# Performance work log

Hardware: AMD Instinct MI355X
Metric: run time of the kernel (lower is better)

The kernel has to match this reference:

```python
import jax, jax.numpy as jnp
import numpy as np
import math


def l1_cdist(a, b):
    """L1 pairwise distance sum_d |a_i - b_j| without materializing (..,n,m,d).
    a: (..., n, d), b: (..., m, d) -> (..., n, m). Scans over feature dim."""
    aT = jnp.moveaxis(a, -1, 0)  # (d, ..., n)
    bT = jnp.moveaxis(b, -1, 0)  # (d, ..., m)
    init = jnp.zeros(a.shape[:-1] + (b.shape[-2],), a.dtype)

    def body(acc, ab):
        ai, bi = ab
        return acc + jnp.abs(ai[..., :, None] - bi[..., None, :]), None

    return jax.lax.scan(body, init, (aT, bT))[0]


def sq_l2_cdist(a, b):
    """Squared euclidean pairwise distance via GEMM (matches cdist(p=2)**2, clamped >=0)."""
    a2 = jnp.sum(a * a, axis=-1)
    b2 = jnp.sum(b * b, axis=-1)
    ab = jnp.einsum('...nd,...md->...nm', a, b)
    return jnp.maximum(a2[..., :, None] + b2[..., None, :] - 2.0 * ab, 0.0)


def proxy_delta_linear(x, weight, gain):
    """ProxyDeltaLinearV68 forward. x: (B,T,Din), weight: (Dout,Din), gain: (1,Dout,1)."""
    B, T, Din = x.shape
    Dout = weight.shape[0]
    x_act = jnp.tanh(x).reshape(-1, Din)   # (B*T, Din)
    w_act = jnp.tanh(weight)               # (Dout, Din)
    l1_mean = jax.lax.stop_gradient(l1_cdist(x_act, w_act)) / Din
    l2_sq_mean = sq_l2_cdist(x_act, w_act) / Din
    # (l1 - l2).detach() + l2
    dist = jax.lax.stop_gradient(l1_mean - l2_sq_mean) + l2_sq_mean
    out = (1.0 - dist).reshape(B, T, Dout)
    return (out - 0.5) * gain.reshape(1, 1, Dout)


def attention_forward(x, mask, wq_weight, wq_gain, wk_weight, wk_gain,
                      wv_weight, wv_gain, wo_weight, wo_bias, gamma, rho):
    B, T, C = x.shape
    H = gamma.shape[1]
    d = C // H
    scale = math.sqrt(d)

    q = jnp.tanh(proxy_delta_linear(x, wq_weight, wq_gain))
    k = jnp.tanh(proxy_delta_linear(x, wk_weight, wk_gain))
    v = proxy_delta_linear(x, wv_weight, wv_gain)

    q = q.reshape(B, T, H, d).transpose(0, 2, 1, 3).reshape(B * H, T, d)
    k = k.reshape(B, T, H, d).transpose(0, 2, 1, 3).reshape(B * H, T, d)
    v = v.reshape(B, T, H, d).transpose(0, 2, 1, 3)  # (B,H,T,d)

    l1_mean = jax.lax.stop_gradient(l1_cdist(q, k)) / d       # (B*H,T,T)
    l2_sq_mean = sq_l2_cdist(q, k) / d
    dist_proxy = jax.lax.stop_gradient(l1_mean - l2_sq_mean) + l2_sq_mean
    dist_proxy = dist_proxy.reshape(B, H, T, T)

    dist_scaled = dist_proxy * scale
    dist_final_sq = dist_scaled * dist_scaled
    gamma_pos = jax.nn.softplus(gamma)  # (1,H,1,1)
    rho_pos = jax.nn.softplus(rho)
    base_kernel = 1.0 / (1.0 + gamma_pos * dist_final_sq + 1e-6)
    attn_weights = base_kernel ** rho_pos
    attn_weights = jnp.where(mask == 0, 0.0, attn_weights)
    attn_probs = attn_weights / (jnp.sum(attn_weights, axis=-1, keepdims=True) + 1e-6)

    out = jnp.einsum('bhqk,bhkd->bhqd', attn_probs, v)
    out = out.transpose(0, 2, 1, 3).reshape(B, T, C)
    return out @ wo_weight.T + wo_bias


def setup_inputs() -> dict:
    B, T, C, H = 2, 2048, 512, 8
    key = jax.random.key(0)
    ks = jax.random.split(key, 8)
    x = jax.random.normal(ks[0], (B, T, C), dtype=jnp.float32)
    mask = jnp.tril(jnp.ones((T, T), dtype=jnp.int32))[None, None]  # causal (1,1,T,T)
    mk = lambda k: jax.random.normal(k, (C, C), dtype=jnp.float32) * 0.1
    return {
        'x': x,
        'mask': mask,
        'wq_weight': mk(ks[1]), 'wq_gain': jnp.full((1, C, 1), 2.0, jnp.float32),
        'wk_weight': mk(ks[2]), 'wk_gain': jnp.full((1, C, 1), 2.0, jnp.float32),
        'wv_weight': mk(ks[3]), 'wv_gain': jnp.full((1, C, 1), 2.0, jnp.float32),
        'wo_weight': jax.random.normal(ks[4], (C, C), dtype=jnp.float32) * (1.0 / math.sqrt(C)),
        'wo_bias': jnp.zeros((C,), dtype=jnp.float32),
        'gamma': jnp.ones((1, H, 1, 1), dtype=jnp.float32),
        'rho': jnp.full((1, H, 1, 1), 2.0, jnp.float32),
    }


def reference(x, mask, wq_weight, wq_gain, wk_weight, wk_gain,
              wv_weight, wv_gain, wo_weight, wo_bias, gamma, rho):
    return attention_forward(x, mask, wq_weight, wq_gain, wk_weight, wk_gain,
                             wv_weight, wv_gain, wo_weight, wo_bias, gamma, rho)
```

## Files before the change

kernel.cpp:

```cpp
#include <hip/hip_runtime.h>
#include <hip/hip_bf16.h>

#define T_SEQ 2048
#define CDIM 512
#define HDIM 8
#define DHEAD 64
#define BT 4096

__global__ __launch_bounds__(256) void tanh_prep(
    const float* __restrict__ x,  const float* __restrict__ wq,
    const float* __restrict__ wk, const float* __restrict__ wv,
    float* __restrict__ xact, float* __restrict__ wqa,
    float* __restrict__ wka,  float* __restrict__ wva)
{
    const int NX = BT * CDIM / 4;
    const int NW = CDIM * CDIM / 4;
    int idx = blockIdx.x * 256 + threadIdx.x;
    const float4* src; float4* dst; int off;
    if (idx < NX)           { src = (const float4*)x;  dst = (float4*)xact; off = idx; }
    else if (idx < NX+NW)   { src = (const float4*)wq; dst = (float4*)wqa;  off = idx - NX; }
    else if (idx < NX+2*NW) { src = (const float4*)wk; dst = (float4*)wka;  off = idx - NX - NW; }
    else                    { src = (const float4*)wv; dst = (float4*)wva;  off = idx - NX - 2*NW; }
    float4 t = src[off];
    t.x = tanhf(t.x); t.y = tanhf(t.y); t.z = tanhf(t.z); t.w = tanhf(t.w);
    dst[off] = t;
}

#define PSTR 36
__global__ __launch_bounds__(256) void proj_l1(
    const float* __restrict__ xact,
    const float* __restrict__ wqa, const float* __restrict__ wka, const float* __restrict__ wva,
    const float* __restrict__ gq,  const float* __restrict__ gk,  const float* __restrict__ gv,
    float* __restrict__ oq, float* __restrict__ okk, float* __restrict__ ov)
{
    __shared__ float As[64][PSTR];
    __shared__ float Bs[128][PSTR];

    const int z = blockIdx.z;
    const float* w    = (z == 0) ? wqa : (z == 1) ? wka : wva;
    const float* gain = (z == 0) ? gq  : (z == 1) ? gk  : gv;
    float* outp       = (z == 0) ? oq  : (z == 1) ? okk : ov;

    const int row0 = blockIdx.y * 64;
    const int col0 = blockIdx.x * 128;
    const int tid = threadIdx.x;
    const int tx = tid & 15, ty = tid >> 4;

    float acc[4][8];
    #pragma unroll
    for (int i = 0; i < 4; ++i)
        #pragma unroll
        for (int j = 0; j < 8; ++j) acc[i][j] = 0.f;

    for (int k0 = 0; k0 < CDIM; k0 += 32) {
        float4 av[2], bv[4];
        #pragma unroll
        for (int q = 0; q < 2; ++q) {
            const int fi = tid + 256 * q;
            av[q] = *(const float4*)&xact[(size_t)(row0 + (fi >> 3)) * CDIM + k0 + 4*(fi & 7)];
        }
        #pragma unroll
        for (int q = 0; q < 4; ++q) {
            const int fi = tid + 256 * q;
            bv[q] = *(const float4*)&w[(size_t)(col0 + (fi >> 3)) * CDIM + k0 + 4*(fi & 7)];
        }
        __syncthreads();
        #pragma unroll
        for (int q = 0; q < 2; ++q) {
            const int fi = tid + 256 * q;
            *(float4*)&As[fi >> 3][4*(fi & 7)] = av[q];
        }
        #pragma unroll
        for (int q = 0; q < 4; ++q) {
            const int fi = tid + 256 * q;
            *(float4*)&Bs[fi >> 3][4*(fi & 7)] = bv[q];
        }
        __syncthreads();

        #pragma unroll 2
        for (int kk = 0; kk < 32; kk += 4) {
            float4 a4[4], b4[8];
            #pragma unroll
            for (int i = 0; i < 4; ++i) a4[i] = *(const float4*)&As[ty + 16*i][kk];
            #pragma unroll
            for (int j = 0; j < 8; ++j) b4[j] = *(const float4*)&Bs[tx + 16*j][kk];
            #pragma unroll
            for (int i = 0; i < 4; ++i)
                #pragma unroll
                for (int j = 0; j < 8; ++j)
                    acc[i][j] += fabsf(a4[i].x - b4[j].x) + fabsf(a4[i].y - b4[j].y)
                               + fabsf(a4[i].z - b4[j].z) + fabsf(a4[i].w - b4[j].w);
        }
        __syncthreads();
    }

    float gcol[8];
    #pragma unroll
    for (int j = 0; j < 8; ++j) gcol[j] = gain[col0 + tx + 16*j];

    #pragma unroll
    for (int i = 0; i < 4; ++i) {
        const int r = row0 + ty + 16*i;
        #pragma unroll
        for (int j = 0; j < 8; ++j) {
            const int c = col0 + tx + 16*j;
            float val = (0.5f - acc[i][j] * (1.0f / 512.0f)) * gcol[j];
            if (z < 2) val = tanhf(val);
            outp[(size_t)r * CDIM + c] = val;
        }
    }
}

__global__ __launch_bounds__(256) void attn_l1(
    const float* __restrict__ qg, const float* __restrict__ kg, const float* __restrict__ vg,
    const float* __restrict__ gamma, const float* __restrict__ rho,
    float* __restrict__ slabv, float* __restrict__ slabs)
{
    __shared__ float Qs[128][68];
    __shared__ float Ks[128][68];
    __shared__ float Vs[128][68];
    __shared__ float Ws[128][36];

    const int bh = blockIdx.x;
    const int b = bh >> 3, h = bh & 7;

    int slot = blockIdx.y;
    int s = 15, c = 0;
    for (;; --s) {
        const int nc = (s >> 2) + 1;
        if (slot < nc) { c = slot; break; }
        slot -= nc;
    }
    const int i0 = s * 128;
    const int kt0 = 4 * c;
    const int kt1 = min(4 * c + 3, s);

    const int tid = threadIdx.x;
    const int tx = tid & 15, ty = tid >> 4;
    const int gr = tid >> 3;
    const int gc = (tid & 7) * 4;

    const float gp = log1pf(__expf(gamma[h]));
    const float rp = log1pf(__expf(rho[h]));
    const float gp64 = gp * (1.0f / 64.0f);
    const float mrho = -rp;

    const size_t hb = (size_t)b * T_SEQ * CDIM + h * DHEAD;

    #pragma unroll
    for (int p = 0; p < 4; ++p)
        #pragma unroll
        for (int h2 = 0; h2 < 2; ++h2)
            *(float4*)&Qs[gr + 32*p][gc + 32*h2] =
                *(const float4*)&qg[hb + (size_t)(i0 + gr + 32*p) * CDIM + gc + 32*h2];

    float4 o4[8];
    float accs[8];
    float l1w[8][8];
    #pragma unroll
    for (int i = 0; i < 8; ++i) {
        o4[i] = make_float4(0.f, 0.f, 0.f, 0.f);
        accs[i] = 0.f;
    }

    for (int kt = kt0; kt <= kt1; ++kt) {
        const int j0 = kt * 128;
        __syncthreads();
        #pragma unroll
        for (int p = 0; p < 4; ++p)
            #pragma unroll
            for (int h2 = 0; h2 < 2; ++h2) {
                const size_t off = hb + (size_t)(j0 + gr + 32*p) * CDIM + gc + 32*h2;
                *(float4*)&Ks[gr + 32*p][gc + 32*h2] = *(const float4*)&kg[off];
                *(float4*)&Vs[gr + 32*p][gc + 32*h2] = *(const float4*)&vg[off];
            }
        __syncthreads();

        #pragma unroll
        for (int i = 0; i < 8; ++i)
            #pragma unroll
            for (int j = 0; j < 8; ++j) l1w[i][j] = 0.f;

        #pragma unroll 2
        for (int d0 = 0; d0 < DHEAD; d0 += 4) {
            float4 a4[8];
            #pragma unroll
            for (int i = 0; i < 8; ++i) a4[i] = *(const float4*)&Qs[ty + 16*i][d0];
            #pragma unroll
            for (int j = 0; j < 8; ++j) {
                const float4 kx = *(const float4*)&Ks[tx + 16*j][d0];
                #pragma unroll
                for (int i = 0; i < 8; ++i)
                    l1w[i][j] += fabsf(a4[i].x - kx.x) + fabsf(a4[i].y - kx.y)
                               + fabsf(a4[i].z - kx.z) + fabsf(a4[i].w - kx.w);
            }
        }

        const bool diag = (kt == s);
        #pragma unroll
        for (int i = 0; i < 8; ++i)
            #pragma unroll
            for (int j = 0; j < 8; ++j) {
                const float l1 = l1w[i][j];
                const float den = fmaf(gp64 * l1, l1, 1.000001f);
                float wgt = __builtin_amdgcn_exp2f(mrho * __builtin_amdgcn_logf(den));
                if (diag && (tx + 16*j) > (ty + 16*i)) wgt = 0.f;
                l1w[i][j] = wgt;
                accs[i] += wgt;
            }

        #pragma unroll
        for (int qtr = 0; qtr < 4; ++qtr) {
            __syncthreads();
            #pragma unroll
            for (int i = 0; i < 8; ++i) {
                Ws[ty + 16*i][tx]      = l1w[i][2*qtr];
                Ws[ty + 16*i][tx + 16] = l1w[i][2*qtr + 1];
            }
            __syncthreads();

            #pragma unroll 2
            for (int jc = 0; jc < 32; jc += 4) {
                float4 w4[8], v4[4];
                #pragma unroll
                for (int i = 0; i < 8; ++i) w4[i] = *(const float4*)&Ws[ty + 16*i][jc];
                #pragma unroll
                for (int jj = 0; jj < 4; ++jj)
                    v4[jj] = *(const float4*)&Vs[qtr*32 + jc + jj][tx*4];
                #pragma unroll
                for (int i = 0; i < 8; ++i) {
                    o4[i].x += w4[i].x*v4[0].x + w4[i].y*v4[1].x + w4[i].z*v4[2].x + w4[i].w*v4[3].x;
                    o4[i].y += w4[i].x*v4[0].y + w4[i].y*v4[1].y + w4[i].z*v4[2].y + w4[i].w*v4[3].y;
                    o4[i].z += w4[i].x*v4[0].z + w4[i].y*v4[1].z + w4[i].z*v4[2].z + w4[i].w*v4[3].z;
                    o4[i].w += w4[i].x*v4[0].w + w4[i].y*v4[1].w + w4[i].z*v4[2].w + w4[i].w*v4[3].w;
                }
            }
        }
    }

    #pragma unroll
    for (int i = 0; i < 8; ++i) {
        accs[i] += __shfl_xor(accs[i], 1, 64);
        accs[i] += __shfl_xor(accs[i], 2, 64);
        accs[i] += __shfl_xor(accs[i], 4, 64);
        accs[i] += __shfl_xor(accs[i], 8, 64);
    }

    float* sv = slabv + (size_t)c * ((size_t)BT * CDIM);
    float* ss = slabs + (size_t)c * ((size_t)BT * HDIM);
    #pragma unroll
    for (int i = 0; i < 8; ++i) {
        const int qr = i0 + ty + 16*i;
        if (tx == 0)
            ss[(size_t)(b * T_SEQ + qr) * HDIM + h] = accs[i];
        *(float4*)&sv[hb + (size_t)qr * CDIM + tx*4] = o4[i];
    }
}

__global__ __launch_bounds__(256) void normalize_k(
    const float* __restrict__ slabv, const float* __restrict__ slabs,
    float* __restrict__ ab)
{
    int idx = blockIdx.x * 256 + threadIdx.x;
    const int row = idx >> 7;
    const int col = (idx & 127) << 2;
    const int h = col >> 6;
    const int t = row & (T_SEQ - 1);
    const int nch = ((t >> 7) >> 2) + 1;

    const size_t NV = (size_t)BT * CDIM / 4;
    const size_t NS = (size_t)BT * HDIM;
    float4 v = ((const float4*)slabv)[idx];
    float ssum = slabs[(size_t)row * HDIM + h];
    #pragma unroll
    for (int c = 1; c < 4; ++c) {
        if (c < nch) {
            float4 u = ((const float4*)slabv)[c * NV + idx];
            v.x += u.x; v.y += u.y; v.z += u.z; v.w += u.w;
            ssum += slabs[c * NS + (size_t)row * HDIM + h];
        }
    }
    const float inv = 1.0f / (ssum + 1e-6f);
    v.x *= inv; v.y *= inv; v.z *= inv; v.w *= inv;
    ((float4*)ab)[idx] = v;
}

__global__ __launch_bounds__(256) void out_gemm(
    const float* __restrict__ A, const float* __restrict__ wo,
    const float* __restrict__ bias, float* __restrict__ Y)
{
    __shared__ float As[128][PSTR];
    __shared__ float Bs[64][PSTR];

    const int row0 = blockIdx.y * 128;
    const int col0 = blockIdx.x * 64;
    const int tid = threadIdx.x;
    const int tx = tid & 15, ty = tid >> 4;
    const int lr = tid >> 3;
    const int lc = (tid & 7) * 4;

    float acc[8][4];
    #pragma unroll
    for (int i = 0; i < 8; ++i)
        #pragma unroll
        for (int j = 0; j < 4; ++j) acc[i][j] = 0.f;

    for (int k0 = 0; k0 < CDIM; k0 += 32) {
        float4 ar[4];
        #pragma unroll
        for (int p = 0; p < 4; ++p)
            ar[p] = *(const float4*)&A[(size_t)(row0 + lr + 32*p) * CDIM + k0 + lc];
        float4 b0 = *(const float4*)&wo[(size_t)(col0 + lr)      * CDIM + k0 + lc];
        float4 b1 = *(const float4*)&wo[(size_t)(col0 + lr + 32) * CDIM + k0 + lc];
        __syncthreads();
        #pragma unroll
        for (int p = 0; p < 4; ++p)
            *(float4*)&As[lr + 32*p][lc] = ar[p];
        *(float4*)&Bs[lr][lc]      = b0;
        *(float4*)&Bs[lr + 32][lc] = b1;
        __syncthreads();

        #pragma unroll
        for (int kk = 0; kk < 32; kk += 4) {
            float4 a4[8], b4[4];
            #pragma unroll
            for (int i = 0; i < 8; ++i) a4[i] = *(const float4*)&As[ty + 16*i][kk];
            #pragma unroll
            for (int j = 0; j < 4; ++j) b4[j] = *(const float4*)&Bs[tx + 16*j][kk];
            #pragma unroll
            for (int i = 0; i < 8; ++i)
                #pragma unroll
                for (int j = 0; j < 4; ++j)
                    acc[i][j] += a4[i].x * b4[j].x + a4[i].y * b4[j].y
                               + a4[i].z * b4[j].z + a4[i].w * b4[j].w;
        }
    }

    float bcol[4];
    #pragma unroll
    for (int j = 0; j < 4; ++j) bcol[j] = bias[col0 + tx + 16*j];

    #pragma unroll
    for (int i = 0; i < 8; ++i) {
        const int r = row0 + ty + 16*i;
        #pragma unroll
        for (int j = 0; j < 4; ++j) {
            const int c = col0 + tx + 16*j;
            Y[(size_t)r * CDIM + c] = acc[i][j] + bcol[j];
        }
    }
}

extern "C" void kernel_launch(void* const* d_in, const int* in_sizes, int n_in,
                              void* d_out, int out_size, void* d_ws, size_t ws_size,
                              hipStream_t stream)
{
    (void)in_sizes; (void)n_in; (void)out_size; (void)ws_size;
    const float* x     = (const float*)d_in[0];
    const float* wq    = (const float*)d_in[2];
    const float* gq    = (const float*)d_in[3];
    const float* wk    = (const float*)d_in[4];
    const float* gk    = (const float*)d_in[5];
    const float* wv    = (const float*)d_in[6];
    const float* gv    = (const float*)d_in[7];
    const float* wo    = (const float*)d_in[8];
    const float* wob   = (const float*)d_in[9];
    const float* gamma = (const float*)d_in[10];
    const float* rho   = (const float*)d_in[11];
    float* out = (float*)d_out;

    const size_t NV = (size_t)BT * CDIM;
    const size_t NW = (size_t)CDIM * CDIM;
    const size_t NS = (size_t)BT * HDIM;

    float* ws    = (float*)d_ws;
    float* xact  = ws;
    float* wqa   = xact + NV;
    float* wka   = wqa + NW;
    float* wva   = wka + NW;
    float* qb    = wva + NW;
    float* kb    = qb + NV;
    float* vb    = kb + NV;
    float* slabv = vb + NV;
    float* slabs = slabv + 4 * NV;
    float* ab    = qb;

    tanh_prep<<<2816, 256, 0, stream>>>(x, wq, wk, wv, xact, wqa, wka, wva);
    proj_l1<<<dim3(4, 64, 3), 256, 0, stream>>>(xact, wqa, wka, wva,
                                                gq, gk, gv, qb, kb, vb);
    attn_l1<<<dim3(16, 40), 256, 0, stream>>>(qb, kb, vb, gamma, rho, slabv, slabs);
    normalize_k<<<2048, 256, 0, stream>>>(slabv, slabs, ab);
    out_gemm<<<dim3(8, 32), 256, 0, stream>>>(ab, wo, wob, out);
}
```

Measured before the change: 674.3 us.

## Halve key tile to 64, alias K/W smem, prefetch next tile into registers

The attention L1 kernel now processes 64-key tiles instead of 128. K and the weight scratch share one shared-memory buffer, which shrinks LDS use, and launch bounds request 2 blocks per SM to raise occupancy. The next K/V tile is loaded into registers while the current tile is computed, so global loads overlap compute. The trade-off is twice as many iterations and barriers per chunk, a finer diagonal mask check, and more register pressure from the prefetch buffers.

```diff
diff --git a/kernel.cpp b/kernel.cpp
--- a/kernel.cpp
+++ b/kernel.cpp
@@ -111,15 +111,14 @@
     }
 }
 
-__global__ __launch_bounds__(256) void attn_l1(
+__global__ __launch_bounds__(256, 2) void attn_l1(
     const float* __restrict__ qg, const float* __restrict__ kg, const float* __restrict__ vg,
     const float* __restrict__ gamma, const float* __restrict__ rho,
     float* __restrict__ slabv, float* __restrict__ slabs)
 {
     __shared__ float Qs[128][68];
-    __shared__ float Ks[128][68];
-    __shared__ float Vs[128][68];
-    __shared__ float Ws[128][36];
+    __shared__ float Vs[64][68];
+    __shared__ float KW[4608];
 
     const int bh = blockIdx.x;
     const int b = bh >> 3, h = bh & 7;
@@ -132,13 +131,11 @@
         slot -= nc;
     }
     const int i0 = s * 128;
-    const int kt0 = 4 * c;
-    const int kt1 = min(4 * c + 3, s);
+    const int kt0 = 8 * c;
+    const int kt1 = min(8 * c + 7, 2 * s + 1);
 
     const int tid = threadIdx.x;
     const int tx = tid & 15, ty = tid >> 4;
-    const int gr = tid >> 3;
-    const int gc = (tid & 7) * 4;
 
     const float gp = log1pf(__expf(gamma[h]));
     const float rp = log1pf(__expf(rho[h]));
@@ -147,16 +144,32 @@
 
     const size_t hb = (size_t)b * T_SEQ * CDIM + h * DHEAD;
 
-    #pragma unroll
-    for (int p = 0; p < 4; ++p)
-        #pragma unroll
-        for (int h2 = 0; h2 < 2; ++h2)
-            *(float4*)&Qs[gr + 32*p][gc + 32*h2] =
-                *(const float4*)&qg[hb + (size_t)(i0 + gr + 32*p) * CDIM + gc + 32*h2];
+    {
+        const int gr = tid >> 3;
+        const int gc = (tid & 7) * 4;
+        #pragma unroll
+        for (int p = 0; p < 4; ++p)
+            #pragma unroll
+            for (int h2 = 0; h2 < 2; ++h2)
+                *(float4*)&Qs[gr + 32*p][gc + 32*h2] =
+                    *(const float4*)&qg[hb + (size_t)(i0 + gr + 32*p) * CDIM + gc + 32*h2];
+    }
+
+    float4 kpre[4], vpre[4];
+    {
+        const int j0 = kt0 * 64;
+        #pragma unroll
+        for (int q = 0; q < 4; ++q) {
+            const int fi = tid + 256 * q;
+            const size_t off = hb + (size_t)(j0 + (fi >> 4)) * CDIM + 4 * (fi & 15);
+            kpre[q] = *(const float4*)&kg[off];
+            vpre[q] = *(const float4*)&vg[off];
+        }
+    }
 
     float4 o4[8];
     float accs[8];
-    float l1w[8][8];
+    float l1w[8][4];
     #pragma unroll
     for (int i = 0; i < 8; ++i) {
         o4[i] = make_float4(0.f, 0.f, 0.f, 0.f);
@@ -164,22 +177,31 @@
     }
 
     for (int kt = kt0; kt <= kt1; ++kt) {
-        const int j0 = kt * 128;
-        __syncthreads();
-        #pragma unroll
-        for (int p = 0; p < 4; ++p)
-            #pragma unroll
-            for (int h2 = 0; h2 < 2; ++h2) {
-                const size_t off = hb + (size_t)(j0 + gr + 32*p) * CDIM + gc + 32*h2;
-                *(float4*)&Ks[gr + 32*p][gc + 32*h2] = *(const float4*)&kg[off];
-                *(float4*)&Vs[gr + 32*p][gc + 32*h2] = *(const float4*)&vg[off];
-            }
+        __syncthreads();
+        {
+            #pragma unroll
+            for (int q = 0; q < 4; ++q) {
+                const int fi = tid + 256 * q;
+                const int r = fi >> 4, c4 = 4 * (fi & 15);
+                *(float4*)&KW[r * 68 + c4] = kpre[q];
+                *(float4*)&Vs[r][c4]       = vpre[q];
+            }
+            const int nkt = (kt + 1 <= kt1) ? kt + 1 : kt1;
+            const int nj0 = nkt * 64;
+            #pragma unroll
+            for (int q = 0; q < 4; ++q) {
+                const int fi = tid + 256 * q;
+                const size_t off = hb + (size_t)(nj0 + (fi >> 4)) * CDIM + 4 * (fi & 15);
+                kpre[q] = *(const float4*)&kg[off];
+                vpre[q] = *(const float4*)&vg[off];
+            }
+        }
         __syncthreads();
 
         #pragma unroll
         for (int i = 0; i < 8; ++i)
             #pragma unroll
-            for (int j = 0; j < 8; ++j) l1w[i][j] = 0.f;
+            for (int j = 0; j < 4; ++j) l1w[i][j] = 0.f;
 
         #pragma unroll 2
         for (int d0 = 0; d0 < DHEAD; d0 += 4) {
@@ -187,8 +209,8 @@
             #pragma unroll
             for (int i = 0; i < 8; ++i) a4[i] = *(const float4*)&Qs[ty + 16*i][d0];
             #pragma unroll
-            for (int j = 0; j < 8; ++j) {
-                const float4 kx = *(const float4*)&Ks[tx + 16*j][d0];
+            for (int j = 0; j < 4; ++j) {
+                const float4 kx = *(const float4*)&KW[(tx + 16*j) * 68 + d0];
                 #pragma unroll
                 for (int i = 0; i < 8; ++i)
                     l1w[i][j] += fabsf(a4[i].x - kx.x) + fabsf(a4[i].y - kx.y)
@@ -196,26 +218,27 @@
             }
         }
 
-        const bool diag = (kt == s);
+        const int j0 = kt * 64;
+        const bool diag = (kt >= 2 * s);
         #pragma unroll
         for (int i = 0; i < 8; ++i)
             #pragma unroll
-            for (int j = 0; j < 8; ++j) {
+            for (int j = 0; j < 4; ++j) {
                 const float l1 = l1w[i][j];
                 const float den = fmaf(gp64 * l1, l1, 1.000001f);
                 float wgt = __builtin_amdgcn_exp2f(mrho * __builtin_amdgcn_logf(den));
-                if (diag && (tx + 16*j) > (ty + 16*i)) wgt = 0.f;
+                if (diag && (j0 + tx + 16*j) > (i0 + ty + 16*i)) wgt = 0.f;
                 l1w[i][j] = wgt;
                 accs[i] += wgt;
             }
 
         #pragma unroll
-        for (int qtr = 0; qtr < 4; ++qtr) {
+        for (int hh = 0; hh < 2; ++hh) {
             __syncthreads();
             #pragma unroll
             for (int i = 0; i < 8; ++i) {
-                Ws[ty + 16*i][tx]      = l1w[i][2*qtr];
-                Ws[ty + 16*i][tx + 16] = l1w[i][2*qtr + 1];
+                KW[(ty + 16*i) * 36 + tx]      = l1w[i][2*hh];
+                KW[(ty + 16*i) * 36 + tx + 16] = l1w[i][2*hh + 1];
             }
             __syncthreads();
 
@@ -223,10 +246,11 @@
             for (int jc = 0; jc < 32; jc += 4) {
                 float4 w4[8], v4[4];
                 #pragma unroll
-                for (int i = 0; i < 8; ++i) w4[i] = *(const float4*)&Ws[ty + 16*i][jc];
+                for (int i = 0; i < 8; ++i)
+                    w4[i] = *(const float4*)&KW[(ty + 16*i) * 36 + jc];
                 #pragma unroll
                 for (int jj = 0; jj < 4; ++jj)
-                    v4[jj] = *(const float4*)&Vs[qtr*32 + jc + jj][tx*4];
+                    v4[jj] = *(const float4*)&Vs[32*hh + jc + jj][tx*4];
                 #pragma unroll
                 for (int i = 0; i < 8; ++i) {
                     o4[i].x += w4[i].x*v4[0].x + w4[i].y*v4[1].x + w4[i].z*v4[2].x + w4[i].w*v4[3].x;
```

After: 637.7 us. 5.4% less time.
